# Optimization experiments

Hardware: AMD Instinct MI355X
Metric: run time of the kernel (lower is better)

The kernel has to match this reference:

```python
import jax, jax.numpy as jnp
import numpy as np

N = 131072        # total nodes
D = 256           # d_model (params.emb_dim)
STEPS = 16        # depth steps
G = N // STEPS    # nodes per depth step (equal-sized groups)
B = 16            # batch (number of trees); all lengths equal N//B
V = 1024          # len(id2word)
# op schedule: -1 leaf embedding, -2 numeric encoder, 0/1 unary ('sin','cos'), 2/3 binary ('add','mul')
SCHEDULE = [-1, -2, 0, 2, 1, 3, 0, 2, 1, 3, 0, 2, 1, 3, 0, 2]


def setup_inputs() -> dict:
    key = jax.random.key(0)
    ks = jax.random.split(key, 8)
    tokens = jax.random.randint(ks[0], (N,), 0, V, dtype=jnp.int32)
    # children of a node at depth d must already be computed: indices < d*G
    rng = np.random.default_rng(0)
    li = np.zeros(N, np.int32)
    ri = np.zeros(N, np.int32)
    for d in range(2, STEPS):
        li[d * G:(d + 1) * G] = rng.integers(0, d * G, G)
        ri[d * G:(d + 1) * G] = rng.integers(0, d * G, G)
    depths = jnp.repeat(jnp.arange(STEPS, dtype=jnp.int32), G)
    operation_order = jnp.array(SCHEDULE, dtype=jnp.int32)
    lengths = jnp.full((B,), N // B, dtype=jnp.int32)
    s = 0.05
    leaf_table = jax.random.normal(ks[1], (V, D), jnp.float32)
    num_W1 = jax.random.normal(ks[2], (D, 1), jnp.float32) * s
    num_b1 = jnp.zeros((D,), jnp.float32)
    num_W2 = jax.random.normal(ks[3], (D, D), jnp.float32) * s
    num_b2 = jnp.zeros((D,), jnp.float32)
    una_W = jax.random.normal(ks[4], (2, 4, D, D), jnp.float32) * s
    una_b = jnp.zeros((2, 4, D), jnp.float32)
    bin_W = jax.random.normal(ks[5], (2, 10, D, D), jnp.float32) * s
    bin_b = jnp.zeros((2, 5, D), jnp.float32)
    return dict(tokens=tokens, left_idx=jnp.asarray(li), right_idx=jnp.asarray(ri),
                depths=depths, operation_order=operation_order, lengths=lengths,
                leaf_table=leaf_table, num_W1=num_W1, num_b1=num_b1,
                num_W2=num_W2, num_b2=num_b2,
                una_W=una_W, una_b=una_b, bin_W=bin_W, bin_b=bin_b)


def _unary_cell(hc, W, b):
    # hc: [G, 2, D]; W: [4, D, D] (data, forget, output, input); b: [4, D]
    h, c = hc[:, 0], hc[:, 1]
    g = jnp.einsum('nd,ked->kne', h, W) + b[:, None, :]  # y = h @ W_k.T + b_k
    i = jax.nn.sigmoid(g[0])
    f = jax.nn.sigmoid(g[1])
    o = jax.nn.sigmoid(g[2])
    u = jnp.tanh(g[3])
    c2 = i * u + f * c
    h2 = o * jnp.tanh(c2)
    h2 = h2 / jnp.linalg.norm(h2)  # global (Frobenius) norm, as in torch h.norm(p=2)
    c2 = c2 / jnp.linalg.norm(c2)
    return jnp.stack([h2, c2], axis=1)


def _binary_cell(hcl, hcr, W, b):
    # W: [10, D, D] = (data_l, data_r, f_ll, f_lr, f_rl, f_rr, out_l, out_r, in_l, in_r)
    # b: [5, D] = (data, forget_l, forget_r, output, input)
    hl, cl = hcl[:, 0], hcl[:, 1]
    hr, cr = hcr[:, 0], hcr[:, 1]
    gl = jnp.einsum('nd,ked->kne', hl, W[jnp.array([0, 2, 4, 6, 8])])
    gr = jnp.einsum('nd,ked->kne', hr, W[jnp.array([1, 3, 5, 7, 9])])
    g = gl + gr + b[:, None, :]
    i = jax.nn.sigmoid(g[0])
    f_l = jax.nn.sigmoid(g[1])
    f_r = jax.nn.sigmoid(g[2])
    o = jax.nn.sigmoid(g[3])
    u = jnp.tanh(g[4])
    c2 = i * u + f_l * cl + f_r * cr
    h2 = o * jnp.tanh(c2)
    h2 = h2 / jnp.linalg.norm(h2)
    c2 = c2 / jnp.linalg.norm(c2)
    return jnp.stack([h2, c2], axis=1)


def reference(tokens, left_idx, right_idx, depths, operation_order, lengths,
              leaf_table, num_W1, num_b1, num_W2, num_b2,
              una_W, una_b, bin_W, bin_b):
    sched = np.asarray(operation_order).tolist()  # static dispatch schedule
    n = tokens.shape[0]
    steps = len(sched)
    g = n // steps
    d_model = leaf_table.shape[1]
    acts = jnp.zeros((n, 2, d_model), leaf_table.dtype)
    for d, op in enumerate(sched):
        s = d * g
        if op == -1:  # leaf embedding with max_norm=1.0 renorm (non-differentiable scale)
            e = leaf_table[tokens[s:s + g]]
            nrm = jnp.linalg.norm(e, axis=-1, keepdims=True)
            scale = jax.lax.stop_gradient(jnp.minimum(1.0, 1.0 / (nrm + 1e-7)))
            e = e * scale
            step_act = jnp.stack([e, jnp.zeros_like(e)], axis=1)
        elif op == -2:  # numeric encoder
            x = tokens[s:s + g].astype(leaf_table.dtype)[:, None]
            h1 = jax.nn.sigmoid(x @ num_W1.T + num_b1)
            e = jax.nn.sigmoid(h1 @ num_W2.T + num_b2)
            step_act = jnp.stack([e, jnp.zeros_like(e)], axis=1)
        elif op in (0, 1):  # unary LSTM cell: gather child then cell
            child = acts[left_idx[s:s + g]]
            step_act = _unary_cell(child, una_W[op], una_b[op])
        else:  # binary LSTM cell: gather both children
            l = acts[left_idx[s:s + g]]
            r = acts[right_idx[s:s + g]]
            step_act = _binary_cell(l, r, bin_W[op - 2], bin_b[op - 2])
        acts = jax.lax.dynamic_update_slice(acts, step_act, (s, 0, 0))
    hidden = acts[:, 0, :]  # [N, D]
    batch = lengths.shape[0]
    # all lengths equal -> pad_sequence is a reshape: [B, L, D]
    return hidden.reshape(batch, n // batch, d_model)
```

## Files before the change

kernel.cpp:

```cpp
#include <hip/hip_runtime.h>
#include <hip/hip_bf16.h>
#include <cstdint>

typedef unsigned short u16;
typedef unsigned int u32;
typedef __attribute__((ext_vector_type(4))) float floatx4;
typedef __attribute__((ext_vector_type(8))) short shortx8;

#define G_STEP 8192
#define N_TOTAL 131072
#define RHALF (1280*256)

__device__ __forceinline__ float bfu2f(u16 x){ return __uint_as_float(((unsigned)x)<<16); }
__device__ __forceinline__ u16 f2bfu(float x){ __hip_bfloat16 b = __float2bfloat16(x); return *reinterpret_cast<u16*>(&b); }
__device__ __forceinline__ float sigm(float x){ return 1.0f/(1.0f+__expf(-x)); }
__device__ __forceinline__ float tanh_(float x){
  float cx = fminf(fmaxf(x,-15.f),15.f);
  float e = __expf(2.f*cx);
  return (e-1.f)/(e+1.f);
}
__device__ __forceinline__ float invs(float x){ return 1.0f/sqrtf(x); }

__device__ __forceinline__ void gl16(const void* g, void* l){
  __builtin_amdgcn_global_load_lds((const __attribute__((address_space(1))) u32*)g,
                                   (__attribute__((address_space(3))) u32*)l, 16, 0, 0);
}

template<int V> __device__ __forceinline__ void wait_vm();
template<> __device__ __forceinline__ void wait_vm<0>(){ asm volatile("s_waitcnt vmcnt(0)" ::: "memory"); }
template<> __device__ __forceinline__ void wait_vm<6>(){ asm volatile("s_waitcnt vmcnt(6)" ::: "memory"); }
template<> __device__ __forceinline__ void wait_vm<7>(){ asm volatile("s_waitcnt vmcnt(7)" ::: "memory"); }
__device__ __forceinline__ void wait_lgkm0(){ asm volatile("s_waitcnt lgkmcnt(0)" ::: "memory"); }

__device__ __forceinline__ void cvt8(const float* __restrict__ src, u16* __restrict__ dst){
  float4 a = *reinterpret_cast<const float4*>(src);
  float4 b = *reinterpret_cast<const float4*>(src+4);
  ushort4 o0; o0.x=f2bfu(a.x); o0.y=f2bfu(a.y); o0.z=f2bfu(a.z); o0.w=f2bfu(a.w);
  ushort4 o1; o1.x=f2bfu(b.x); o1.y=f2bfu(b.y); o1.z=f2bfu(b.z); o1.w=f2bfu(b.w);
  *reinterpret_cast<ushort4*>(dst)   = o0;
  *reinterpret_cast<ushort4*>(dst+4) = o1;
}

__global__ __launch_bounds__(256) void setup_kernel(
    const int* __restrict__ tokens, const float* __restrict__ leaf_table,
    const float* __restrict__ W1, const float* __restrict__ b1,
    const float* __restrict__ una_W, const float* __restrict__ bin_W,
    const float* __restrict__ num_W2,
    u16* __restrict__ wbu, u16* __restrict__ wbb, u16* __restrict__ wbn,
    u16* __restrict__ h1, u16* __restrict__ H, u16* __restrict__ C,
    float* __restrict__ sumsq)
{
  const int b = blockIdx.x, tid = threadIdx.x;
  if (b < 256){
    int row = b*8 + (tid>>5), d0 = (tid&31)*8;
    int op = row>>10, w = row&1023;
    int gate = (w>>4)&3, e = ((w>>6)<<4) | (w&15);
    cvt8(una_W + (size_t)((op*4+gate)*256 + e)*256 + d0, wbu + (size_t)row*256 + d0);
  } else if (b < 896){
    int row = (b-256)*8 + (tid>>5), d0 = (tid&31)*8;
    int ob = row / 2560, rem = row - ob*2560;
    int lr = rem / 1280, rw = rem - lr*1280;
    int eblk = rw / 80, rem2 = rw - eblk*80;
    int gate = rem2 >> 4, el = rem2 & 15;
    int e = eblk*16 + el;
    cvt8(bin_W + (size_t)((ob*10 + 2*gate + lr)*256 + e)*256 + d0, wbb + (size_t)row*256 + d0);
  } else if (b < 928){
    int row = (b-896)*8 + (tid>>5), d0 = (tid&31)*8;
    cvt8(num_W2 + (size_t)row*256 + d0, wbn + (size_t)row*256 + d0);
  } else if (b < 2976){
    int wave = tid >> 6, lane = tid & 63;
    int node = (b-928)*4 + wave;
    int t = tokens[node];
    const float4 e4 = *reinterpret_cast<const float4*>(leaf_table + (size_t)t*256 + lane*4);
    float ss = e4.x*e4.x + e4.y*e4.y + e4.z*e4.z + e4.w*e4.w;
    #pragma unroll
    for (int o = 32; o; o >>= 1) ss += __shfl_down(ss, o);
    ss = __shfl(ss, 0);
    float scale = fminf(1.0f, 1.0f/(sqrtf(ss) + 1e-7f));
    ushort4 hv;
    hv.x = f2bfu(e4.x*scale); hv.y = f2bfu(e4.y*scale);
    hv.z = f2bfu(e4.z*scale); hv.w = f2bfu(e4.w*scale);
    ushort4 zv; zv.x = zv.y = zv.z = zv.w = 0;
    *reinterpret_cast<ushort4*>(H + (size_t)node*256 + lane*4) = hv;
    *reinterpret_cast<ushort4*>(C + (size_t)node*256 + lane*4) = zv;
  } else if (b < 4000){
    int flat = (b-2976)*2048 + tid*8;
    int n = flat >> 8, d0 = flat & 255;
    float x = (float)tokens[G_STEP + n];
    float4 w0 = *reinterpret_cast<const float4*>(W1 + d0);
    float4 w1 = *reinterpret_cast<const float4*>(W1 + d0 + 4);
    float4 c0 = *reinterpret_cast<const float4*>(b1 + d0);
    float4 c1 = *reinterpret_cast<const float4*>(b1 + d0 + 4);
    ushort4 o0, o1;
    o0.x = f2bfu(sigm(x*w0.x + c0.x)); o0.y = f2bfu(sigm(x*w0.y + c0.y));
    o0.z = f2bfu(sigm(x*w0.z + c0.z)); o0.w = f2bfu(sigm(x*w0.w + c0.w));
    o1.x = f2bfu(sigm(x*w1.x + c1.x)); o1.y = f2bfu(sigm(x*w1.y + c1.y));
    o1.z = f2bfu(sigm(x*w1.z + c1.z)); o1.w = f2bfu(sigm(x*w1.w + c1.w));
    *reinterpret_cast<ushort4*>(h1 + flat)     = o0;
    *reinterpret_cast<ushort4*>(h1 + flat + 4) = o1;
  } else {
    if (tid < 32) sumsq[tid] = ((tid & 15) < 2) ? 1.0f : 0.0f;
  }
}

template<int MODE>
__global__ __launch_bounds__(512, 2) void gemm_fused(
    const u16* __restrict__ Asrc, const int* __restrict__ lidx,
    const int* __restrict__ ridx, const u16* __restrict__ Wb,
    const float* __restrict__ bias, const u16* __restrict__ Cin,
    float* __restrict__ sumsq, u16* __restrict__ H, u16* __restrict__ C,
    int sbase, int step)
{
  constexpr int NG  = (MODE==0) ? 1 : (MODE==1 ? 4 : 5);
  constexpr int NBR = (MODE==2) ? 160 : 128;
  constexpr int NT  = (MODE==2) ? 8 : 4;
  constexpr int WN  = (MODE==2) ? 80 : 64;
  constexpr int NFR = WN/16;
  constexpr int NBG = NBR/8;

  __shared__ u16 SA[2][256][64];
  __shared__ u16 SB[2][NBR][64];
  __shared__ float scH[16];
  __shared__ float scC[16];
  __shared__ float red[16];

  const int tid  = threadIdx.x;
  const int lane = tid & 63, wave = tid >> 6;

  const int bid = blockIdx.x;
  const int jj  = bid >> 3;
  const int bx  = (bid & 7) + 8*(jj & 3);
  const int by  = jj >> 2;
  const int mbase = bx*256;
  const int nbase = by*NBR;

  const int l15 = lane & 15, kg = lane >> 4;
  const int wm = (wave >> 1)*64, wn = (wave & 1)*WN;

  if (MODE != 0){
    if (tid < 16)      scH[tid]    = invs(sumsq[tid]);
    else if (tid < 32) scC[tid-16] = invs(sumsq[tid]);
  }

  const int rhi = lane >> 3;
  const int lc  = (lane & 7) ^ rhi;

  const u16* aL[4]; const u16* aR[4];
  #pragma unroll
  for (int g = 0; g < 4; g++){
    int r = (wave*4 + g)*8 + rhi;
    int gr;
    if constexpr (MODE==0) gr = mbase + r;
    else                   gr = lidx[sbase + mbase + r];
    aL[g] = Asrc + (size_t)gr*256 + lc*8;
    if constexpr (MODE==2)
      aR[g] = Asrc + (size_t)ridx[sbase + mbase + r]*256 + lc*8;
  }
  const int nbg_w = (MODE==2) ? ((wave < 4) ? 3 : 2) : 2;
  const int bg0   = (MODE==2) ? ((wave < 4) ? wave*3 : 12 + (wave-4)*2) : wave*2;
  const u16* bP[3];
  #pragma unroll
  for (int g = 0; g < 3; g++){
    int gg = bg0 + g;
    if (gg >= NBG) gg = NBG-1;
    bP[g] = Wb + (size_t)(nbase + gg*8 + rhi)*256 + lc*8;
  }

  floatx4 accL[4][NFR];
  #pragma unroll
  for (int i = 0; i < 4; i++)
    #pragma unroll
    for (int j2 = 0; j2 < NFR; j2++) accL[i][j2] = (floatx4)(0.0f);
  floatx4 accR[(MODE==2)?4:1][(MODE==2)?NFR:1];
  if constexpr (MODE==2){
    #pragma unroll
    for (int i = 0; i < 4; i++)
      #pragma unroll
      for (int j2 = 0; j2 < NFR; j2++) accR[i][j2] = (floatx4)(0.0f);
  }

  auto stage = [&](int t, int buf){
    const int kk = t*64;
    #pragma unroll
    for (int g = 0; g < 4; g++){
      const u16* ga;
      if constexpr (MODE==2){ ga = (kk >= 256) ? aR[g] + (kk-256) : aL[g] + kk; }
      else                  { ga = aL[g] + kk; }
      gl16(ga, &SA[buf][(wave*4 + g)*8][0]);
    }
    #pragma unroll
    for (int g = 0; g < 3; g++){
      if (g < nbg_w){
        const u16* gb;
        if constexpr (MODE==2){ gb = (kk >= 256) ? bP[g] + RHALF + (kk-256) : bP[g] + kk; }
        else                  { gb = bP[g] + kk; }
        gl16(gb, &SB[buf][(bg0 + g)*8][0]);
      }
    }
  };

  stage(0, 0);
  stage(1, 1);
  if (MODE==2 && wave < 4) asm volatile("s_waitcnt vmcnt(7) lgkmcnt(0)" ::: "memory");
  else                     asm volatile("s_waitcnt vmcnt(6) lgkmcnt(0)" ::: "memory");
  __builtin_amdgcn_s_barrier();

  #pragma unroll
  for (int t = 0; t < NT; t++){
    const int buf = t & 1;
    {
      shortx8 af[4], bfr[NFR];
      const int pc = (kg ^ (l15 & 7)) * 8;
      #pragma unroll
      for (int i = 0; i < 4; i++)
        af[i] = *reinterpret_cast<const shortx8*>(&SA[buf][wm + i*16 + l15][pc]);
      #pragma unroll
      for (int n = 0; n < NFR; n++)
        bfr[n] = *reinterpret_cast<const shortx8*>(&SB[buf][wn + n*16 + l15][pc]);
      if (MODE==2 && t >= 4){
        #pragma unroll
        for (int mi = 0; mi < 4; mi++)
          #pragma unroll
          for (int ni = 0; ni < NFR; ni++)
            accR[mi][ni] = __builtin_amdgcn_mfma_f32_16x16x32_bf16(af[mi], bfr[ni], accR[mi][ni], 0, 0, 0);
      } else {
        #pragma unroll
        for (int mi = 0; mi < 4; mi++)
          #pragma unroll
          for (int ni = 0; ni < NFR; ni++)
            accL[mi][ni] = __builtin_amdgcn_mfma_f32_16x16x32_bf16(af[mi], bfr[ni], accL[mi][ni], 0, 0, 0);
      }
    }
    {
      shortx8 af[4], bfr[NFR];
      const int pc = ((4 + kg) ^ (l15 & 7)) * 8;
      #pragma unroll
      for (int i = 0; i < 4; i++)
        af[i] = *reinterpret_cast<const shortx8*>(&SA[buf][wm + i*16 + l15][pc]);
      #pragma unroll
      for (int n = 0; n < NFR; n++)
        bfr[n] = *reinterpret_cast<const shortx8*>(&SB[buf][wn + n*16 + l15][pc]);
      wait_lgkm0();
      __builtin_amdgcn_s_barrier();
      if (t + 2 < NT) stage(t+2, buf);
      if (MODE==2 && t >= 4){
        #pragma unroll
        for (int mi = 0; mi < 4; mi++)
          #pragma unroll
          for (int ni = 0; ni < NFR; ni++)
            accR[mi][ni] = __builtin_amdgcn_mfma_f32_16x16x32_bf16(af[mi], bfr[ni], accR[mi][ni], 0, 0, 0);
      } else {
        #pragma unroll
        for (int mi = 0; mi < 4; mi++)
          #pragma unroll
          for (int ni = 0; ni < NFR; ni++)
            accL[mi][ni] = __builtin_amdgcn_mfma_f32_16x16x32_bf16(af[mi], bfr[ni], accL[mi][ni], 0, 0, 0);
      }
    }
    if (t + 1 < NT){
      if (t + 2 < NT){
        if (MODE==2 && wave < 4) wait_vm<7>(); else wait_vm<6>();
      } else wait_vm<0>();
      __builtin_amdgcn_s_barrier();
    }
  }

  if constexpr (MODE == 0){
    float bb[4];
    #pragma unroll
    for (int ni = 0; ni < 4; ni++) bb[ni] = bias[nbase + wn + ni*16 + l15];
    #pragma unroll
    for (int mi = 0; mi < 4; mi++){
      #pragma unroll
      for (int r = 0; r < 4; r++){
        int node = sbase + mbase + wm + mi*16 + kg*4 + r;
        u16* hp = H + (size_t)node*256 + nbase + wn + l15;
        u16* cp = C + (size_t)node*256 + nbase + wn + l15;
        #pragma unroll
        for (int ni = 0; ni < 4; ni++){
          hp[ni*16] = f2bfu(sigm(accL[mi][ni][r] + bb[ni]));
          cp[ni*16] = 0;
        }
      }
    }
  } else {
    const int eb = by*2 + (wave & 1);
    const int e  = eb*16 + l15;
    float bb[NG];
    #pragma unroll
    for (int g = 0; g < NG; g++) bb[g] = bias[g*256 + e];
    float hss = 0.f, css = 0.f;
    #pragma unroll
    for (int mi = 0; mi < 4; mi++){
      #pragma unroll
      for (int r = 0; r < 4; r++){
        int orow = mbase + wm + mi*16 + kg*4 + r;
        int node = sbase + orow;
        int chl = lidx[node];
        float sl = scH[chl >> 13];
        float cl = bfu2f(Cin[(size_t)chl*256 + e]) * scC[chl >> 13];
        float c2, h2;
        if constexpr (MODE == 1){
          float i_ = sigm(accL[mi][0][r]*sl + bb[0]);
          float f_ = sigm(accL[mi][1][r]*sl + bb[1]);
          float o_ = sigm(accL[mi][2][r]*sl + bb[2]);
          float u_ = tanh_(accL[mi][3][r]*sl + bb[3]);
          c2 = i_*u_ + f_*cl;
          h2 = o_*tanh_(c2);
        } else {
          int chr = ridx[node];
          float sr = scH[chr >> 13];
          float cr = bfu2f(Cin[(size_t)chr*256 + e]) * scC[chr >> 13];
          float g0 = accL[mi][0][r]*sl + accR[mi][0][r]*sr + bb[0];
          float g1 = accL[mi][1][r]*sl + accR[mi][1][r]*sr + bb[1];
          float g2 = accL[mi][2][r]*sl + accR[mi][2][r]*sr + bb[2];
          float g3 = accL[mi][3][r]*sl + accR[mi][3][r]*sr + bb[3];
          float g4 = accL[mi][4][r]*sl + accR[mi][4][r]*sr + bb[4];
          float i_ = sigm(g0);
          float fl = sigm(g1);
          float fr = sigm(g2);
          float o_ = sigm(g3);
          float u_ = tanh_(g4);
          c2 = i_*u_ + fl*cl + fr*cr;
          h2 = o_*tanh_(c2);
        }
        H[(size_t)node*256 + e] = f2bfu(h2);
        C[(size_t)node*256 + e] = f2bfu(c2);
        hss += h2*h2;
        css += c2*c2;
      }
    }
    #pragma unroll
    for (int o = 32; o; o >>= 1){ hss += __shfl_down(hss, o); css += __shfl_down(css, o); }
    if (lane == 0){ red[wave] = hss; red[8+wave] = css; }
    __syncthreads();
    if (tid == 0){
      float s = 0.f;
      #pragma unroll
      for (int w = 0; w < 8; w++) s += red[w];
      atomicAdd(&sumsq[step], s);
    }
    if (tid == 64){
      float s = 0.f;
      #pragma unroll
      for (int w = 0; w < 8; w++) s += red[8+w];
      atomicAdd(&sumsq[16 + step], s);
    }
  }
}

__global__ __launch_bounds__(256) void out_kernel(
    const u16* __restrict__ H, const float* __restrict__ sumsq, float* __restrict__ out)
{
  size_t base = ((size_t)blockIdx.x*256 + threadIdx.x)*8;
  int n = (int)(base >> 8);
  float s = invs(sumsq[n >> 13]);
  const uint4 v = *reinterpret_cast<const uint4*>(H + base);
  float4 o0, o1;
  o0.x = bfu2f((u16)(v.x & 0xffff))*s; o0.y = bfu2f((u16)(v.x >> 16))*s;
  o0.z = bfu2f((u16)(v.y & 0xffff))*s; o0.w = bfu2f((u16)(v.y >> 16))*s;
  o1.x = bfu2f((u16)(v.z & 0xffff))*s; o1.y = bfu2f((u16)(v.z >> 16))*s;
  o1.z = bfu2f((u16)(v.w & 0xffff))*s; o1.w = bfu2f((u16)(v.w >> 16))*s;
  *reinterpret_cast<float4*>(out + base)     = o0;
  *reinterpret_cast<float4*>(out + base + 4) = o1;
}

extern "C" void kernel_launch(void* const* d_in, const int* in_sizes, int n_in,
                              void* d_out, int out_size, void* d_ws, size_t ws_size,
                              hipStream_t stream)
{
  const int*   tokens     = (const int*)d_in[0];
  const int*   lidx       = (const int*)d_in[1];
  const int*   ridx       = (const int*)d_in[2];
  const float* leaf_table = (const float*)d_in[6];
  const float* num_W1     = (const float*)d_in[7];
  const float* num_b1     = (const float*)d_in[8];
  const float* num_W2     = (const float*)d_in[9];
  const float* num_b2     = (const float*)d_in[10];
  const float* una_W      = (const float*)d_in[11];
  const float* una_b      = (const float*)d_in[12];
  const float* bin_W      = (const float*)d_in[13];
  const float* bin_b      = (const float*)d_in[14];

  char* ws = (char*)d_ws;
  size_t off = 0;
  u16* H   = (u16*)(ws + off); off += (size_t)N_TOTAL*256*2;
  u16* wbu = (u16*)(ws + off); off += (size_t)2048*256*2;
  u16* wbb = (u16*)(ws + off); off += (size_t)5120*256*2;
  u16* wbn = (u16*)(ws + off); off += (size_t)256*256*2;
  u16* h1  = (u16*)(ws + off); off += (size_t)G_STEP*256*2;
  float* sumsq = (float*)(ws + off); off += 32*4;

  u16* C = (u16*)d_out;

  setup_kernel<<<4001, 256, 0, stream>>>(tokens, leaf_table, num_W1, num_b1,
                                         una_W, bin_W, num_W2,
                                         wbu, wbb, wbn, h1, H, C, sumsq);
  gemm_fused<0><<<64, 512, 0, stream>>>(
      h1, nullptr, nullptr, wbn, num_b2, nullptr, sumsq, H, C, G_STEP, 1);

  const int sched[16] = {-1,-2,0,2,1,3,0,2,1,3,0,2,1,3,0,2};
  for (int d = 2; d < 16; d++){
    int op = sched[d];
    int sbase = d*G_STEP;
    if (op == 0 || op == 1){
      gemm_fused<1><<<256, 512, 0, stream>>>(
          H, lidx, nullptr, wbu + (size_t)op*1024*256,
          una_b + (size_t)op*4*256, C, sumsq, H, C, sbase, d);
    } else {
      int o2 = op - 2;
      gemm_fused<2><<<256, 512, 0, stream>>>(
          H, lidx, ridx, wbb + (size_t)o2*2*1280*256,
          bin_b + (size_t)o2*5*256, C, sumsq, H, C, sbase, d);
    }
  }
  out_kernel<<<(N_TOTAL*256)/(256*8), 256, 0, stream>>>(H, sumsq, (float*)d_out);
}
```

Measured before the change: 373.4 us.

## Triple-buffer LDS staging in fused GEMM to drop the mid-iteration barrier

The A and B shared-memory tiles go from double to triple buffering. The prefetch for step t+2 is now issued at the start of each k-iteration instead of after a mid-iteration barrier, which removes one barrier and one lgkm wait per iteration. The intent is better overlap of global-to-LDS loads with MFMA work. The cost is roughly 50% more LDS per block, which likely drops the kernel from two resident blocks per CU to one and so reduces occupancy and latency hiding.

```diff
diff --git a/kernel.cpp b/kernel.cpp
--- a/kernel.cpp
+++ b/kernel.cpp
@@ -26,11 +26,10 @@
                                    (__attribute__((address_space(3))) u32*)l, 16, 0, 0);
 }
 
-template<int V> __device__ __forceinline__ void wait_vm();
-template<> __device__ __forceinline__ void wait_vm<0>(){ asm volatile("s_waitcnt vmcnt(0)" ::: "memory"); }
-template<> __device__ __forceinline__ void wait_vm<6>(){ asm volatile("s_waitcnt vmcnt(6)" ::: "memory"); }
-template<> __device__ __forceinline__ void wait_vm<7>(){ asm volatile("s_waitcnt vmcnt(7)" ::: "memory"); }
-__device__ __forceinline__ void wait_lgkm0(){ asm volatile("s_waitcnt lgkmcnt(0)" ::: "memory"); }
+template<int V> __device__ __forceinline__ void wait_vml();
+template<> __device__ __forceinline__ void wait_vml<0>(){ asm volatile("s_waitcnt vmcnt(0) lgkmcnt(0)" ::: "memory"); }
+template<> __device__ __forceinline__ void wait_vml<6>(){ asm volatile("s_waitcnt vmcnt(6) lgkmcnt(0)" ::: "memory"); }
+template<> __device__ __forceinline__ void wait_vml<7>(){ asm volatile("s_waitcnt vmcnt(7) lgkmcnt(0)" ::: "memory"); }
 
 __device__ __forceinline__ void cvt8(const float* __restrict__ src, u16* __restrict__ dst){
   float4 a = *reinterpret_cast<const float4*>(src);
@@ -118,8 +117,8 @@
   constexpr int NFR = WN/16;
   constexpr int NBG = NBR/8;
 
-  __shared__ u16 SA[2][256][64];
-  __shared__ u16 SB[2][NBR][64];
+  __shared__ u16 SA[3][256][64];
+  __shared__ u16 SB[3][NBR][64];
   __shared__ float scH[16];
   __shared__ float scC[16];
   __shared__ float red[16];
@@ -179,14 +178,15 @@
       for (int j2 = 0; j2 < NFR; j2++) accR[i][j2] = (floatx4)(0.0f);
   }
 
-  auto stage = [&](int t, int buf){
+  auto stage = [&](int t){
+    const int slot = t % 3;
     const int kk = t*64;
     #pragma unroll
     for (int g = 0; g < 4; g++){
       const u16* ga;
       if constexpr (MODE==2){ ga = (kk >= 256) ? aR[g] + (kk-256) : aL[g] + kk; }
       else                  { ga = aL[g] + kk; }
-      gl16(ga, &SA[buf][(wave*4 + g)*8][0]);
+      gl16(ga, &SA[slot][(wave*4 + g)*8][0]);
     }
     #pragma unroll
     for (int g = 0; g < 3; g++){
@@ -194,29 +194,30 @@
         const u16* gb;
         if constexpr (MODE==2){ gb = (kk >= 256) ? bP[g] + RHALF + (kk-256) : bP[g] + kk; }
         else                  { gb = bP[g] + kk; }
-        gl16(gb, &SB[buf][(bg0 + g)*8][0]);
+        gl16(gb, &SB[slot][(bg0 + g)*8][0]);
       }
     }
   };
 
-  stage(0, 0);
-  stage(1, 1);
-  if (MODE==2 && wave < 4) asm volatile("s_waitcnt vmcnt(7) lgkmcnt(0)" ::: "memory");
-  else                     asm volatile("s_waitcnt vmcnt(6) lgkmcnt(0)" ::: "memory");
+  stage(0);
+  stage(1);
+  if (MODE==2 && wave < 4) wait_vml<7>(); else wait_vml<6>();
   __builtin_amdgcn_s_barrier();
 
   #pragma unroll
   for (int t = 0; t < NT; t++){
-    const int buf = t & 1;
+    const int slot = t % 3;
+    if (t + 2 < NT) stage(t+2);
+
     {
       shortx8 af[4], bfr[NFR];
       const int pc = (kg ^ (l15 & 7)) * 8;
       #pragma unroll
       for (int i = 0; i < 4; i++)
-        af[i] = *reinterpret_cast<const shortx8*>(&SA[buf][wm + i*16 + l15][pc]);
+        af[i] = *reinterpret_cast<const shortx8*>(&SA[slot][wm + i*16 + l15][pc]);
       #pragma unroll
       for (int n = 0; n < NFR; n++)
-        bfr[n] = *reinterpret_cast<const shortx8*>(&SB[buf][wn + n*16 + l15][pc]);
+        bfr[n] = *reinterpret_cast<const shortx8*>(&SB[slot][wn + n*16 + l15][pc]);
       if (MODE==2 && t >= 4){
         #pragma unroll
         for (int mi = 0; mi < 4; mi++)
@@ -236,13 +237,10 @@
       const int pc = ((4 + kg) ^ (l15 & 7)) * 8;
       #pragma unroll
       for (int i = 0; i < 4; i++)
-        af[i] = *reinterpret_cast<const shortx8*>(&SA[buf][wm + i*16 + l15][pc]);
+        af[i] = *reinterpret_cast<const shortx8*>(&SA[slot][wm + i*16 + l15][pc]);
       #pragma unroll
       for (int n = 0; n < NFR; n++)
-        bfr[n] = *reinterpret_cast<const shortx8*>(&SB[buf][wn + n*16 + l15][pc]);
-      wait_lgkm0();
-      __builtin_amdgcn_s_barrier();
-      if (t + 2 < NT) stage(t+2, buf);
+        bfr[n] = *reinterpret_cast<const shortx8*>(&SB[slot][wn + n*16 + l15][pc]);
       if (MODE==2 && t >= 4){
         #pragma unroll
         for (int mi = 0; mi < 4; mi++)
@@ -257,10 +255,11 @@
             accL[mi][ni] = __builtin_amdgcn_mfma_f32_16x16x32_bf16(af[mi], bfr[ni], accL[mi][ni], 0, 0, 0);
       }
     }
+
     if (t + 1 < NT){
       if (t + 2 < NT){
-        if (MODE==2 && wave < 4) wait_vm<7>(); else wait_vm<6>();
-      } else wait_vm<0>();
+        if (MODE==2 && wave < 4) wait_vml<7>(); else wait_vml<6>();
+      } else wait_vml<0>();
       __builtin_amdgcn_s_barrier();
     }
   }
```

New measurement: 362.5 us. 2.9% less time.
